# Optimization experiments

Hardware: AMD Instinct MI355X
Metric: run time of the kernel (lower is better)

The kernel has to match this reference:

```python
import jax, jax.numpy as jnp
import numpy as np

B, H, W, C = 16, 256, 256, 16
HO, WO = 256, 256


def setup_inputs() -> dict:
    key = jax.random.key(0)
    k1, k2 = jax.random.split(key)
    x = jax.random.normal(k1, (B, H, W, C), dtype=jnp.float32)
    # loc network: global avg pool -> dense(C, 6); small weights, identity bias
    W_loc = jax.random.normal(k2, (C, 6), dtype=jnp.float32) * 0.01
    b_loc = jnp.asarray([1.0, 0.0, 0.0, 1.0, 0.0, 0.0], dtype=jnp.float32)
    # coords_grid = np.indices(output_grid_shape): (2, HO, WO), [0]=row idx, [1]=col idx
    coords_grid = jnp.asarray(np.indices((HO, WO), dtype=np.float32))
    return {"x": x, "W_loc": W_loc, "b_loc": b_loc, "coords_grid": coords_grid}


def _forward(x, W_loc, b_loc, coords_grid):
    # loc network: predict 6 affine params per batch element
    pooled = jnp.mean(x, axis=(1, 2))              # [B, C]
    params = pooled @ W_loc + b_loc                # [B, 6]
    A = params[:, :4].reshape(-1, 2, 2)            # [B, 2, 2]
    t = params[:, 4:]                              # [B, 2]
    # grid_transform_fn: affine map of pixel coordinates
    tc = jnp.einsum('bij,jhw->bihw', A, coords_grid) + t[:, :, None, None]  # [B,2,HO,WO]
    yc, xc = tc[:, 0], tc[:, 1]                    # [B, HO, WO] each
    # interpolation_fn: bilinear sampling with clipping (wrap=False)
    y0 = jnp.floor(yc)
    x0 = jnp.floor(xc)
    wy = yc - y0                                   # fractional weights
    wx = xc - x0
    y0i = jnp.clip(y0.astype(jnp.int32), 0, H - 1)
    y1i = jnp.clip(y0.astype(jnp.int32) + 1, 0, H - 1)
    x0i = jnp.clip(x0.astype(jnp.int32), 0, W - 1)
    x1i = jnp.clip(x0.astype(jnp.int32) + 1, 0, W - 1)
    bidx = jnp.arange(x.shape[0])[:, None, None]   # [B,1,1] batch gather index
    Ia = x[bidx, y0i, x0i]                         # [B,HO,WO,C]
    Ib = x[bidx, y0i, x1i]
    Ic = x[bidx, y1i, x0i]
    Id = x[bidx, y1i, x1i]
    wa = ((1.0 - wy) * (1.0 - wx))[..., None]
    wb = ((1.0 - wy) * wx)[..., None]
    wc = (wy * (1.0 - wx))[..., None]
    wd = (wy * wx)[..., None]
    return wa * Ia + wb * Ib + wc * Ic + wd * Id   # [B,HO,WO,C]


def reference(x, W_loc, b_loc, coords_grid):
    return _forward(x, W_loc, b_loc, coords_grid)
```

## Files before the change

### kernel.cpp

```cpp
#include <hip/hip_runtime.h>

#define BB 16
#define HH 256
#define WW 256
#define CC 16
#define NPIX (HH * WW)
#define SLICES 128
#define POOL_BLOCKS (BB * SLICES)

__global__ __launch_bounds__(256) void pool_partial(const float4* __restrict__ x4,
                                                    float4* __restrict__ part) {
    const int blk = blockIdx.x;
    const int tid = threadIdx.x;
    const float4* p = x4 + (size_t)blk * 2048 + tid;
    float4 acc = {0.f, 0.f, 0.f, 0.f};
#pragma unroll
    for (int k = 0; k < 8; ++k) {
        float4 v = p[k * 256];
        acc.x += v.x; acc.y += v.y; acc.z += v.z; acc.w += v.w;
    }
    for (int off = 4; off < 64; off <<= 1) {
        acc.x += __shfl_down(acc.x, off);
        acc.y += __shfl_down(acc.y, off);
        acc.z += __shfl_down(acc.z, off);
        acc.w += __shfl_down(acc.w, off);
    }
    __shared__ float4 wsum[4][4];
    const int wave = tid >> 6, lane = tid & 63;
    if (lane < 4) wsum[wave][lane] = acc;
    __syncthreads();
    if (tid < 4) {
        float4 t0 = wsum[0][tid], t1 = wsum[1][tid];
        float4 t2 = wsum[2][tid], t3 = wsum[3][tid];
        float4 t;
        t.x = t0.x + t1.x + t2.x + t3.x;
        t.y = t0.y + t1.y + t2.y + t3.y;
        t.z = t0.z + t1.z + t2.z + t3.z;
        t.w = t0.w + t1.w + t2.w + t3.w;
        part[blk * 4 + tid] = t;
    }
}

__global__ __launch_bounds__(256) void compute_params(const float* __restrict__ part,
                                                      const float* __restrict__ W_loc,
                                                      const float* __restrict__ b_loc,
                                                      float* __restrict__ params) {
    __shared__ float pooled[BB][CC];
    const int tid = threadIdx.x;
    const int b = tid >> 4;
    const int c = tid & 15;
    const float* q = part + (size_t)b * SLICES * CC + c;
    float s = 0.f;
#pragma unroll 8
    for (int k = 0; k < SLICES; ++k)
        s += q[k * CC];
    pooled[b][c] = s * (1.0f / 65536.0f);
    __syncthreads();
    if (tid < BB * 6) {
        const int bb = tid / 6, j = tid % 6;
        float a = b_loc[j];
#pragma unroll
        for (int cc = 0; cc < CC; ++cc)
            a += pooled[bb][cc] * W_loc[cc * 6 + j];
        params[bb * 6 + j] = a;
    }
}

__global__ __launch_bounds__(256) void sample(
    const float4* __restrict__ x4,
    const float* __restrict__ params,
    float4* __restrict__ out)
{
    const int tid = threadIdx.x;
    const int b   = blockIdx.x >> 10;
    const int pix = ((blockIdx.x & 1023) << 6) + (tid >> 2);
    const int cq  = tid & 3;
    const int h   = pix >> 8;
    const int w   = pix & 255;

    const float* pr = params + b * 6;
    const float p0 = pr[0], p1 = pr[1], p2 = pr[2];
    const float p3 = pr[3], p4 = pr[4], p5 = pr[5];

    const float fh = (float)h, fw = (float)w;
    const float yc = p0 * fh + p1 * fw + p4;
    const float xc = p2 * fh + p3 * fw + p5;

    const float y0f = floorf(yc), x0f = floorf(xc);
    const float wy = yc - y0f, wx = xc - x0f;
    const int y0 = (int)y0f, x0 = (int)x0f;
    const int y0i = min(max(y0, 0), HH - 1);
    const int y1i = min(max(y0 + 1, 0), HH - 1);
    const int x0i = min(max(x0, 0), WW - 1);
    const int x1i = min(max(x0 + 1, 0), WW - 1);

    const size_t base = (size_t)b * NPIX;
    const float4* r0 = x4 + (base + (size_t)y0i * WW) * 4 + cq;
    const float4* r1 = x4 + (base + (size_t)y1i * WW) * 4 + cq;
    const float4 Ia = r0[(size_t)x0i * 4];
    const float4 Ib = r0[(size_t)x1i * 4];
    const float4 Ic = r1[(size_t)x0i * 4];
    const float4 Id = r1[(size_t)x1i * 4];

    const float wa = (1.f - wy) * (1.f - wx);
    const float wb = (1.f - wy) * wx;
    const float wc = wy * (1.f - wx);
    const float wd = wy * wx;

    float4 o;
    o.x = wa * Ia.x + wb * Ib.x + wc * Ic.x + wd * Id.x;
    o.y = wa * Ia.y + wb * Ib.y + wc * Ic.y + wd * Id.y;
    o.z = wa * Ia.z + wb * Ib.z + wc * Ic.z + wd * Id.z;
    o.w = wa * Ia.w + wb * Ib.w + wc * Ic.w + wd * Id.w;

    out[(base + pix) * 4 + cq] = o;
}

extern "C" void kernel_launch(void* const* d_in, const int* in_sizes, int n_in,
                              void* d_out, int out_size, void* d_ws, size_t ws_size,
                              hipStream_t stream) {
    const float* x     = (const float*)d_in[0];
    const float* W_loc = (const float*)d_in[1];
    const float* b_loc = (const float*)d_in[2];

    float* part   = (float*)d_ws;
    float* params = part + POOL_BLOCKS * CC;

    pool_partial<<<POOL_BLOCKS, 256, 0, stream>>>((const float4*)x, (float4*)part);
    compute_params<<<1, 256, 0, stream>>>(part, W_loc, b_loc, params);
    sample<<<BB * 1024, 256, 0, stream>>>((const float4*)x, params, (float4*)d_out);
}
```

Measured before the change: 140.8 us.

## Fuse param computation into sampler and loop 16 pixels per thread

Drops the single-block compute_params launch. Each sampling block now reduces its batch's pool partials and computes the six affine parameters itself in shared memory. The sampler grid shrinks from 16384 to 1024 blocks, and each thread loops over 16 pixels. This removes one launch and its serialization bubble, at the cost of redundant per-block reduction work and fewer blocks to hide gather latency.

```diff
diff --git a/kernel.cpp b/kernel.cpp
--- a/kernel.cpp
+++ b/kernel.cpp
@@ -41,79 +41,99 @@
     }
 }
 
-__global__ __launch_bounds__(256) void compute_params(const float* __restrict__ part,
-                                                      const float* __restrict__ W_loc,
-                                                      const float* __restrict__ b_loc,
-                                                      float* __restrict__ params) {
-    __shared__ float pooled[BB][CC];
-    const int tid = threadIdx.x;
-    const int b = tid >> 4;
-    const int c = tid & 15;
-    const float* q = part + (size_t)b * SLICES * CC + c;
-    float s = 0.f;
-#pragma unroll 8
-    for (int k = 0; k < SLICES; ++k)
-        s += q[k * CC];
-    pooled[b][c] = s * (1.0f / 65536.0f);
-    __syncthreads();
-    if (tid < BB * 6) {
-        const int bb = tid / 6, j = tid % 6;
-        float a = b_loc[j];
-#pragma unroll
-        for (int cc = 0; cc < CC; ++cc)
-            a += pooled[bb][cc] * W_loc[cc * 6 + j];
-        params[bb * 6 + j] = a;
-    }
-}
-
-__global__ __launch_bounds__(256) void sample(
+__global__ __launch_bounds__(256) void sample_fused(
     const float4* __restrict__ x4,
-    const float* __restrict__ params,
+    const float* __restrict__ W_loc,
+    const float* __restrict__ b_loc,
+    const float4* __restrict__ part,
     float4* __restrict__ out)
 {
-    const int tid = threadIdx.x;
-    const int b   = blockIdx.x >> 10;
-    const int pix = ((blockIdx.x & 1023) << 6) + (tid >> 2);
-    const int cq  = tid & 3;
-    const int h   = pix >> 8;
-    const int w   = pix & 255;
+    const int tid  = threadIdx.x;
+    const int blk  = blockIdx.x;
+    const int b    = blk >> 6;
+    const int wave = tid >> 6, lane = tid & 63;
 
-    const float* pr = params + b * 6;
+    __shared__ float4 wsum[4][4];
+    __shared__ float  pooled[CC];
+    __shared__ float  pr[6];
+
+    {
+        const float4* q = part + (size_t)b * 512;
+        float4 a0 = q[tid], a1 = q[tid + 256];
+        float4 acc;
+        acc.x = a0.x + a1.x; acc.y = a0.y + a1.y;
+        acc.z = a0.z + a1.z; acc.w = a0.w + a1.w;
+        for (int off = 4; off < 64; off <<= 1) {
+            acc.x += __shfl_down(acc.x, off);
+            acc.y += __shfl_down(acc.y, off);
+            acc.z += __shfl_down(acc.z, off);
+            acc.w += __shfl_down(acc.w, off);
+        }
+        if (lane < 4) wsum[wave][lane] = acc;
+        __syncthreads();
+        if (tid < 4) {
+            float4 t0 = wsum[0][tid], t1 = wsum[1][tid];
+            float4 t2 = wsum[2][tid], t3 = wsum[3][tid];
+            pooled[tid * 4 + 0] = (t0.x + t1.x + t2.x + t3.x) * (1.0f / 65536.0f);
+            pooled[tid * 4 + 1] = (t0.y + t1.y + t2.y + t3.y) * (1.0f / 65536.0f);
+            pooled[tid * 4 + 2] = (t0.z + t1.z + t2.z + t3.z) * (1.0f / 65536.0f);
+            pooled[tid * 4 + 3] = (t0.w + t1.w + t2.w + t3.w) * (1.0f / 65536.0f);
+        }
+        __syncthreads();
+        if (tid < 6) {
+            float a = b_loc[tid];
+#pragma unroll
+            for (int c = 0; c < CC; ++c)
+                a += pooled[c] * W_loc[c * 6 + tid];
+            pr[tid] = a;
+        }
+        __syncthreads();
+    }
+
     const float p0 = pr[0], p1 = pr[1], p2 = pr[2];
     const float p3 = pr[3], p4 = pr[4], p5 = pr[5];
+    const size_t base    = (size_t)b * NPIX;
+    const int    pixBase = (blk & 63) * 1024 + (tid >> 2);
+    const int    cq      = tid & 3;
 
-    const float fh = (float)h, fw = (float)w;
-    const float yc = p0 * fh + p1 * fw + p4;
-    const float xc = p2 * fh + p3 * fw + p5;
+#pragma unroll 4
+    for (int k = 0; k < 16; ++k) {
+        const int pix = pixBase + k * 64;
+        const int h = pix >> 8;
+        const int w = pix & 255;
 
-    const float y0f = floorf(yc), x0f = floorf(xc);
-    const float wy = yc - y0f, wx = xc - x0f;
-    const int y0 = (int)y0f, x0 = (int)x0f;
-    const int y0i = min(max(y0, 0), HH - 1);
-    const int y1i = min(max(y0 + 1, 0), HH - 1);
-    const int x0i = min(max(x0, 0), WW - 1);
-    const int x1i = min(max(x0 + 1, 0), WW - 1);
+        const float fh = (float)h, fw = (float)w;
+        const float yc = p0 * fh + p1 * fw + p4;
+        const float xc = p2 * fh + p3 * fw + p5;
 
-    const size_t base = (size_t)b * NPIX;
-    const float4* r0 = x4 + (base + (size_t)y0i * WW) * 4 + cq;
-    const float4* r1 = x4 + (base + (size_t)y1i * WW) * 4 + cq;
-    const float4 Ia = r0[(size_t)x0i * 4];
-    const float4 Ib = r0[(size_t)x1i * 4];
-    const float4 Ic = r1[(size_t)x0i * 4];
-    const float4 Id = r1[(size_t)x1i * 4];
+        const float y0f = floorf(yc), x0f = floorf(xc);
+        const float wy = yc - y0f, wx = xc - x0f;
+        const int y0 = (int)y0f, x0 = (int)x0f;
+        const int y0i = min(max(y0, 0), HH - 1);
+        const int y1i = min(max(y0 + 1, 0), HH - 1);
+        const int x0i = min(max(x0, 0), WW - 1);
+        const int x1i = min(max(x0 + 1, 0), WW - 1);
 
-    const float wa = (1.f - wy) * (1.f - wx);
-    const float wb = (1.f - wy) * wx;
-    const float wc = wy * (1.f - wx);
-    const float wd = wy * wx;
+        const float4* r0 = x4 + (base + (size_t)y0i * WW) * 4 + cq;
+        const float4* r1 = x4 + (base + (size_t)y1i * WW) * 4 + cq;
+        const float4 Ia = r0[(size_t)x0i * 4];
+        const float4 Ib = r0[(size_t)x1i * 4];
+        const float4 Ic = r1[(size_t)x0i * 4];
+        const float4 Id = r1[(size_t)x1i * 4];
 
-    float4 o;
-    o.x = wa * Ia.x + wb * Ib.x + wc * Ic.x + wd * Id.x;
-    o.y = wa * Ia.y + wb * Ib.y + wc * Ic.y + wd * Id.y;
-    o.z = wa * Ia.z + wb * Ib.z + wc * Ic.z + wd * Id.z;
-    o.w = wa * Ia.w + wb * Ib.w + wc * Ic.w + wd * Id.w;
+        const float wa = (1.f - wy) * (1.f - wx);
+        const float wb = (1.f - wy) * wx;
+        const float wc = wy * (1.f - wx);
+        const float wd = wy * wx;
 
-    out[(base + pix) * 4 + cq] = o;
+        float4 o;
+        o.x = wa * Ia.x + wb * Ib.x + wc * Ic.x + wd * Id.x;
+        o.y = wa * Ia.y + wb * Ib.y + wc * Ic.y + wd * Id.y;
+        o.z = wa * Ia.z + wb * Ib.z + wc * Ic.z + wd * Id.z;
+        o.w = wa * Ia.w + wb * Ib.w + wc * Ic.w + wd * Id.w;
+
+        out[(base + pix) * 4 + cq] = o;
+    }
 }
 
 extern "C" void kernel_launch(void* const* d_in, const int* in_sizes, int n_in,
@@ -123,10 +143,9 @@
     const float* W_loc = (const float*)d_in[1];
     const float* b_loc = (const float*)d_in[2];
 
-    float* part   = (float*)d_ws;
-    float* params = part + POOL_BLOCKS * CC;
+    float4* part = (float4*)d_ws;
 
-    pool_partial<<<POOL_BLOCKS, 256, 0, stream>>>((const float4*)x, (float4*)part);
-    compute_params<<<1, 256, 0, stream>>>(part, W_loc, b_loc, params);
-    sample<<<BB * 1024, 256, 0, stream>>>((const float4*)x, params, (float4*)d_out);
+    pool_partial<<<POOL_BLOCKS, 256, 0, stream>>>((const float4*)x, part);
+    sample_fused<<<BB * 64, 256, 0, stream>>>((const float4*)x, W_loc, b_loc,
+                                              part, (float4*)d_out);
 }
```

Result: faster. 131.2 us (-6.8%).
